# Kernel optimization log

Hardware: AMD Instinct MI355X
Metric: run time of the kernel (lower is better)

## Reference

```python
import jax, jax.numpy as jnp
import numpy as np

H = 256
EDGE_DIM = 16
B, N = 8, 4096
E = 524288
EPS = 1e-5


def setup_inputs() -> dict:
    key = jax.random.key(0)
    ks = jax.random.split(key, 16)
    s = 0.02
    return {
        "h": jax.random.normal(ks[0], (B, N, H), dtype=jnp.float32),
        "edge_index": jax.random.randint(ks[1], (2, E), 0, B * N, dtype=jnp.int64),
        "edge_attr": jax.random.normal(ks[2], (E, EDGE_DIM), dtype=jnp.float32),
        "mask": jnp.ones((B, N), dtype=jnp.float32),
        # message_net params
        "W1": jax.random.normal(ks[3], (2 * H + EDGE_DIM, H), dtype=jnp.float32) * s,
        "b1": jnp.zeros((H,), dtype=jnp.float32),
        "W2": jax.random.normal(ks[4], (H, H), dtype=jnp.float32) * s,
        "b2": jnp.zeros((H,), dtype=jnp.float32),
        # update_net params
        "U1": jax.random.normal(ks[5], (2 * H, H), dtype=jnp.float32) * s,
        "c1": jnp.zeros((H,), dtype=jnp.float32),
        "U2": jax.random.normal(ks[6], (H, H), dtype=jnp.float32) * s,
        "c2": jnp.zeros((H,), dtype=jnp.float32),
        # LayerNorm params
        "gamma": jnp.ones((H,), dtype=jnp.float32),
        "beta": jnp.zeros((H,), dtype=jnp.float32),
    }


def reference(h, edge_index, edge_attr, mask, W1, b1, W2, b2, U1, c1, U2, c2, gamma, beta):
    batch, n_nodes, hid = h.shape
    h_flat = h.reshape(-1, hid)                       # (B*N, H)
    src, dst = edge_index[0], edge_index[1]
    # gather -> message MLP
    msg_in = jnp.concatenate([h_flat[src], h_flat[dst], edge_attr], axis=-1)  # (E, 2H+16)
    messages = jax.nn.silu(msg_in @ W1 + b1) @ W2 + b2                        # (E, H)
    # scatter-add aggregation by destination node
    aggr = jax.ops.segment_sum(messages, dst, num_segments=batch * n_nodes)   # (B*N, H)
    # update MLP + residual (dropout = identity in eval mode)
    upd_in = jnp.concatenate([h_flat, aggr], axis=-1)                         # (B*N, 2H)
    h_new = h_flat + (jax.nn.silu(upd_in @ U1 + c1) @ U2 + c2)
    # LayerNorm over last dim
    mu = jnp.mean(h_new, axis=-1, keepdims=True)
    var = jnp.mean(jnp.square(h_new - mu), axis=-1, keepdims=True)
    h_new = (h_new - mu) * jax.lax.rsqrt(var + EPS) * gamma + beta
    return h_new.reshape(batch, n_nodes, hid) * mask[..., None]
```

## Files before the change

kernel.cpp:

```cpp
#include <hip/hip_runtime.h>

#define H_DIM 256
#define E_NUM 524288
#define NN    32768
#define K2    512
#define K2S   520
#define SAS   264
#define XS    264
#define NPW   4

typedef unsigned short u16;
typedef unsigned int   u32;
typedef __attribute__((ext_vector_type(8))) short s16x8;
typedef __attribute__((ext_vector_type(4))) float f32x4;
typedef __attribute__((ext_vector_type(2))) float f32x2;
typedef __attribute__((ext_vector_type(4))) unsigned short u16x4;

__device__ __forceinline__ u16 f2b(float x) {
    u32 u = __float_as_uint(x);
    u32 r = (u + 0x7FFFu + ((u >> 16) & 1u)) >> 16;
    return (u16)r;
}
__device__ __forceinline__ float b2f(u16 v) {
    u32 u = ((u32)v) << 16;
    return __uint_as_float(u);
}
__device__ __forceinline__ float fsig(float x) {
    return __builtin_amdgcn_rcpf(1.f + __expf(-x));
}

__global__ __launch_bounds__(256) void k_prep_w(
    const float* __restrict__ W1, const float* __restrict__ W2,
    const float* __restrict__ U1, const float* __restrict__ U2,
    u16* __restrict__ WpqT, u16* __restrict__ W2T,
    u16* __restrict__ U1T, u16* __restrict__ U2T) {
    int idx = blockIdx.x * 256 + threadIdx.x;
    if (idx < 131072) {
        int c = idx >> 8, k = idx & 255;
        float v = (c < 256) ? W1[k * 256 + c] : W1[(256 + k) * 256 + (c - 256)];
        WpqT[idx] = f2b(v);
    } else if (idx < 196608) {
        int i = idx - 131072; int c = i >> 8, k = i & 255;
        W2T[i] = f2b(W2[k * 256 + c]);
    } else if (idx < 327680) {
        int i = idx - 196608; int c = i >> 9, k = i & 511;
        U1T[i] = f2b(U1[(size_t)k * 256 + c]);
    } else if (idx < 393216) {
        int i = idx - 327680; int c = i >> 8, k = i & 255;
        U2T[i] = f2b(U2[k * 256 + c]);
    }
}

__global__ __launch_bounds__(256) void k_hist(const int* __restrict__ eidx,
                                              int* __restrict__ cnt) {
    int i = blockIdx.x * 256 + threadIdx.x;
    if (i < E_NUM) atomicAdd(&cnt[eidx[E_NUM + i]], 1);
}

__global__ __launch_bounds__(256) void k_scan(const int* __restrict__ cnt,
                                              int* __restrict__ base,
                                              int* __restrict__ nxt) {
    __shared__ int wsum[4];
    const int t = threadIdx.x, lane = t & 63, w = t >> 6;
    const int st = t * 128;
    int s = 0;
#pragma unroll 8
    for (int i = 0; i < 128; ++i) s += cnt[st + i];
    int sc = s;
#pragma unroll
    for (int off = 1; off < 64; off <<= 1) {
        int v = __shfl_up(sc, off);
        if (lane >= off) sc += v;
    }
    if (lane == 63) wsum[w] = sc;
    __syncthreads();
    int woff = 0;
    for (int i = 0; i < w; ++i) woff += wsum[i];
    const int excl = woff + sc - s;
    if (t == 255) base[NN] = woff + sc;
    int off = excl;
    for (int i = 0; i < 128; ++i) {
        int v = cnt[st + i];
        base[st + i] = off;
        nxt[st + i] = off;
        off += v;
    }
}

__global__ __launch_bounds__(256) void k_scatter(const int* __restrict__ eidx,
                                                 int* __restrict__ nxt,
                                                 int2* __restrict__ elist) {
    int i = blockIdx.x * 256 + threadIdx.x;
    if (i < E_NUM) {
        int d = eidx[E_NUM + i];
        int p = atomicAdd(&nxt[d], 1);
        elist[p] = make_int2(eidx[i], i);
    }
}

__global__ __launch_bounds__(256, 2) void k_gemm_pq(
    const float* __restrict__ h, const u16* __restrict__ WpqT,
    u16* __restrict__ PQ) {
    __shared__ __align__(16) u16 sA[64 * SAS];
    const int t = threadIdx.x;
    const int rowTile = blockIdx.x >> 1, q = blockIdx.x & 1;
    const int n0 = rowTile * 64;
    {
        const int r = t >> 2, g = t & 3;
        const float* hrow = h + (size_t)(n0 + r) * 256;
        u16* rowp = sA + r * SAS;
#pragma unroll
        for (int j = 0; j < 8; ++j) {
            const int c = g + 4 * j;
            float4 v0 = *reinterpret_cast<const float4*>(hrow + c * 8);
            float4 v1 = *reinterpret_cast<const float4*>(hrow + c * 8 + 4);
            s16x8 o;
            o[0] = (short)f2b(v0.x); o[1] = (short)f2b(v0.y);
            o[2] = (short)f2b(v0.z); o[3] = (short)f2b(v0.w);
            o[4] = (short)f2b(v1.x); o[5] = (short)f2b(v1.y);
            o[6] = (short)f2b(v1.z); o[7] = (short)f2b(v1.w);
            *reinterpret_cast<s16x8*>(rowp + c * 8) = o;
        }
    }
    __syncthreads();
    const int lane = t & 63, wv = t >> 6;
    const int l15 = lane & 15, l4 = lane >> 4;
    const int colBase = wv * 64 + l15;
    const f32x4 z4 = {0.f, 0.f, 0.f, 0.f};
    f32x4 acc[4][4];
#pragma unroll
    for (int m = 0; m < 4; ++m)
#pragma unroll
        for (int n = 0; n < 4; ++n) acc[m][n] = z4;
    {
        const u16* Bb = WpqT + (size_t)(q * 256 + colBase) * 256 + l4 * 8;
        for (int kk = 0; kk < 8; ++kk) {
            s16x8 a[4], b[4];
#pragma unroll
            for (int m = 0; m < 4; ++m)
                a[m] = *reinterpret_cast<const s16x8*>(sA + (m * 16 + l15) * SAS + kk * 32 + l4 * 8);
#pragma unroll
            for (int n = 0; n < 4; ++n)
                b[n] = *reinterpret_cast<const s16x8*>(Bb + (size_t)n * 16 * 256 + kk * 32);
#pragma unroll
            for (int m = 0; m < 4; ++m)
#pragma unroll
                for (int n = 0; n < 4; ++n)
                    acc[m][n] = __builtin_amdgcn_mfma_f32_16x16x32_bf16(a[m], b[n], acc[m][n], 0, 0, 0);
        }
    }
#pragma unroll
    for (int m = 0; m < 4; ++m)
#pragma unroll
        for (int j = 0; j < 4; ++j) {
            const int row = n0 + m * 16 + l4 * 4 + j;
            u16* op = PQ + (size_t)row * 512 + q * 256 + colBase;
#pragma unroll
            for (int n = 0; n < 4; ++n) op[n * 16] = f2b(acc[m][n][j]);
        }
}


#define LDEA(S0, S1, S2, S3, k) do {                                        \
    const int _eid = __builtin_amdgcn_readlane(eeY, (k));                   \
    const float* _ep = ea + (size_t)_eid * 16;                              \
    S0 = *reinterpret_cast<const float4*>(_ep);                             \
    S1 = *reinterpret_cast<const float4*>(_ep + 4);                         \
    S2 = *reinterpret_cast<const float4*>(_ep + 8);                         \
    S3 = *reinterpret_cast<const float4*>(_ep + 12);                        \
} while (0)

__global__ __launch_bounds__(256, 4) void k_aggr(
    const u16* __restrict__ PQ, const int2* __restrict__ elist,
    const int* __restrict__ base, const float* __restrict__ ea,
    const float* __restrict__ W1, const float* __restrict__ b1,
    u16* __restrict__ Sb) {
    const int t = threadIdx.x, lane = t & 63, wv = t >> 6;
    const int c0 = lane * 4;
    f32x2 WrL[16], WrH[16];
#pragma unroll
    for (int k = 0; k < 16; ++k) {
        float4 w = *reinterpret_cast<const float4*>(W1 + (size_t)(512 + k) * 256 + c0);
        WrL[k] = f32x2{w.x, w.y};
        WrH[k] = f32x2{w.z, w.w};
    }
    const float4 b1v = *reinterpret_cast<const float4*>(b1 + c0);

    const int dBase = (blockIdx.x * 4 + wv) * NPW;
    for (int nn = 0; nn < NPW; ++nn) {
        const int d = __builtin_amdgcn_readfirstlane(dBase + nn);
        f32x2 qbL = {b1v.x, b1v.y}, qbH = {b1v.z, b1v.w};
        {
            u16x4 qv = *reinterpret_cast<const u16x4*>(PQ + (size_t)d * 512 + 256 + c0);
            qbL[0] += b2f(qv.x); qbL[1] += b2f(qv.y);
            qbH[0] += b2f(qv.z); qbH[1] += b2f(qv.w);
        }
        const int eBeg = __builtin_amdgcn_readfirstlane(base[d]);
        const int nAll = __builtin_amdgcn_readfirstlane(base[d + 1]) - eBeg;
        f32x2 accL = {0.f, 0.f}, accH = {0.f, 0.f};

        for (int cb = 0; cb < nAll; cb += 64) {
            const int m = min(64, nAll - cb);
            const int2 ee = elist[eBeg + cb + min(lane, m - 1)];
            const int eeX = ee.x, eeY = ee.y;

            auto gather = [&](int idx) -> u16x4 {
                const int s = __builtin_amdgcn_readlane(eeX, idx);
                return *reinterpret_cast<const u16x4*>(PQ + (size_t)s * 512 + c0);
            };
            auto edge_compute = [&](const u16x4& pc, const float4& E0, const float4& E1,
                                    const float4& E2, const float4& E3) {
                f32x2 xL = qbL, xH = qbH;
                xL[0] += b2f(pc.x); xL[1] += b2f(pc.y);
                xH[0] += b2f(pc.z); xH[1] += b2f(pc.w);
                xL = xL + WrL[0]  * E0.x; xH = xH + WrH[0]  * E0.x;
                xL = xL + WrL[1]  * E0.y; xH = xH + WrH[1]  * E0.y;
                xL = xL + WrL[2]  * E0.z; xH = xH + WrH[2]  * E0.z;
                xL = xL + WrL[3]  * E0.w; xH = xH + WrH[3]  * E0.w;
                xL = xL + WrL[4]  * E1.x; xH = xH + WrH[4]  * E1.x;
                xL = xL + WrL[5]  * E1.y; xH = xH + WrH[5]  * E1.y;
                xL = xL + WrL[6]  * E1.z; xH = xH + WrH[6]  * E1.z;
                xL = xL + WrL[7]  * E1.w; xH = xH + WrH[7]  * E1.w;
                xL = xL + WrL[8]  * E2.x; xH = xH + WrH[8]  * E2.x;
                xL = xL + WrL[9]  * E2.y; xH = xH + WrH[9]  * E2.y;
                xL = xL + WrL[10] * E2.z; xH = xH + WrH[10] * E2.z;
                xL = xL + WrL[11] * E2.w; xH = xH + WrH[11] * E2.w;
                xL = xL + WrL[12] * E3.x; xH = xH + WrH[12] * E3.x;
                xL = xL + WrL[13] * E3.y; xH = xH + WrH[13] * E3.y;
                xL = xL + WrL[14] * E3.z; xH = xH + WrH[14] * E3.z;
                xL = xL + WrL[15] * E3.w; xH = xH + WrH[15] * E3.w;
                accL[0] += xL[0] * fsig(xL[0]);
                accL[1] += xL[1] * fsig(xL[1]);
                accH[0] += xH[0] * fsig(xH[0]);
                accH[1] += xH[1] * fsig(xH[1]);
            };

            u16x4 p0 = gather(0), p1 = gather(1), p2 = gather(2), p3 = gather(3);
            float4 A0, A1, A2, A3, B0, B1, B2, B3;
            LDEA(A0, A1, A2, A3, 0);
            LDEA(B0, B1, B2, B3, min(1, 63));
            int kb = 0;
            for (; kb + 4 <= m; kb += 4) {
                edge_compute(p0, A0, A1, A2, A3);
                LDEA(A0, A1, A2, A3, min(kb + 2, 63));
                p0 = gather(min(kb + 4, 63));
                edge_compute(p1, B0, B1, B2, B3);
                LDEA(B0, B1, B2, B3, min(kb + 3, 63));
                p1 = gather(min(kb + 5, 63));
                edge_compute(p2, A0, A1, A2, A3);
                LDEA(A0, A1, A2, A3, min(kb + 4, 63));
                p2 = gather(min(kb + 6, 63));
                edge_compute(p3, B0, B1, B2, B3);
                LDEA(B0, B1, B2, B3, min(kb + 5, 63));
                p3 = gather(min(kb + 7, 63));
            }
            if (kb + 0 < m) edge_compute(p0, A0, A1, A2, A3);
            if (kb + 1 < m) edge_compute(p1, B0, B1, B2, B3);
            if (kb + 2 < m) {
                LDEA(A0, A1, A2, A3, kb + 2);
                edge_compute(p2, A0, A1, A2, A3);
            }
        }
        u16x4 o;
        o.x = f2b(accL[0]); o.y = f2b(accL[1]);
        o.z = f2b(accH[0]); o.w = f2b(accH[1]);
        *reinterpret_cast<u16x4*>(Sb + (size_t)d * 256 + c0) = o;
    }
}

__global__ __launch_bounds__(256, 2) void k_post(
    const float* __restrict__ h, const u16* __restrict__ Sb,
    const u16* __restrict__ W2T, const int* __restrict__ base,
    const float* __restrict__ b2,
    const u16* __restrict__ U1T, const u16* __restrict__ U2T,
    const float* __restrict__ c1, const float* __restrict__ c2,
    const float* __restrict__ gamma, const float* __restrict__ beta,
    const float* __restrict__ mask,
    float* __restrict__ out) {
    __shared__ __align__(16) char smemraw[64 * XS * 4];
    u16* sA = reinterpret_cast<u16*>(smemraw);
    const int t  = threadIdx.x;
    const int n0 = blockIdx.x * 64;

    {
        const int r = t >> 2, g = t & 3;
        const int node = n0 + r;
        const float* hrow = h + (size_t)node * H_DIM;
        const u16* srow = Sb + (size_t)node * H_DIM;
        u16* rowp = sA + r * K2S;
#pragma unroll
        for (int j = 0; j < 16; ++j) {
            const int c = g + 4 * j;
            if (c < 32) {
                float4 v0 = *reinterpret_cast<const float4*>(hrow + c * 8);
                float4 v1 = *reinterpret_cast<const float4*>(hrow + c * 8 + 4);
                s16x8 o;
                o[0] = (short)f2b(v0.x); o[1] = (short)f2b(v0.y);
                o[2] = (short)f2b(v0.z); o[3] = (short)f2b(v0.w);
                o[4] = (short)f2b(v1.x); o[5] = (short)f2b(v1.y);
                o[6] = (short)f2b(v1.z); o[7] = (short)f2b(v1.w);
                *reinterpret_cast<s16x8*>(rowp + c * 8) = o;
            } else {
                const int cc = c - 32;
                *reinterpret_cast<s16x8*>(rowp + 256 + cc * 8) =
                    *reinterpret_cast<const s16x8*>(srow + cc * 8);
            }
        }
    }
    __syncthreads();

    const int lane = t & 63, wv = t >> 6;
    const int l15 = lane & 15, l4 = lane >> 4;
    const int colBase = wv * 64 + l15;
    const f32x4 z4 = {0.f, 0.f, 0.f, 0.f};

    f32x4 acc[4][4];
#pragma unroll
    for (int m = 0; m < 4; ++m)
#pragma unroll
        for (int n = 0; n < 4; ++n) acc[m][n] = z4;

    {
        const u16* Bb = W2T + (size_t)colBase * 256 + l4 * 8;
        for (int kk = 0; kk < 8; ++kk) {
            s16x8 a[4], b[4];
#pragma unroll
            for (int m = 0; m < 4; ++m)
                a[m] = *reinterpret_cast<const s16x8*>(sA + (m * 16 + l15) * K2S + 256 + kk * 32 + l4 * 8);
#pragma unroll
            for (int n = 0; n < 4; ++n)
                b[n] = *reinterpret_cast<const s16x8*>(Bb + (size_t)n * 16 * 256 + kk * 32);
#pragma unroll
            for (int m = 0; m < 4; ++m)
#pragma unroll
                for (int n = 0; n < 4; ++n)
                    acc[m][n] = __builtin_amdgcn_mfma_f32_16x16x32_bf16(a[m], b[n], acc[m][n], 0, 0, 0);
        }
    }
    __syncthreads();

    {
        float b2v[4];
#pragma unroll
        for (int n = 0; n < 4; ++n) b2v[n] = b2[colBase + n * 16];
#pragma unroll
        for (int m = 0; m < 4; ++m)
#pragma unroll
            for (int j = 0; j < 4; ++j) {
                const int row = m * 16 + l4 * 4 + j;
                const float dv = (float)(base[n0 + row + 1] - base[n0 + row]);
#pragma unroll
                for (int n = 0; n < 4; ++n)
                    sA[row * K2S + 256 + colBase + n * 16] = f2b(acc[m][n][j] + dv * b2v[n]);
            }
    }
    __syncthreads();

#pragma unroll
    for (int m = 0; m < 4; ++m)
#pragma unroll
        for (int n = 0; n < 4; ++n) acc[m][n] = z4;
    {
        const u16* Bb = U1T + (size_t)colBase * K2 + l4 * 8;
        for (int kk = 0; kk < 16; ++kk) {
            s16x8 a[4], b[4];
#pragma unroll
            for (int m = 0; m < 4; ++m)
                a[m] = *reinterpret_cast<const s16x8*>(sA + (m * 16 + l15) * K2S + kk * 32 + l4 * 8);
#pragma unroll
            for (int n = 0; n < 4; ++n)
                b[n] = *reinterpret_cast<const s16x8*>(Bb + (size_t)n * 16 * K2 + kk * 32);
#pragma unroll
            for (int m = 0; m < 4; ++m)
#pragma unroll
                for (int n = 0; n < 4; ++n)
                    acc[m][n] = __builtin_amdgcn_mfma_f32_16x16x32_bf16(a[m], b[n], acc[m][n], 0, 0, 0);
        }
    }
    __syncthreads();

    {
        u16* sX = reinterpret_cast<u16*>(smemraw);
        float c1v[4];
#pragma unroll
        for (int n = 0; n < 4; ++n) c1v[n] = c1[colBase + n * 16];
#pragma unroll
        for (int m = 0; m < 4; ++m)
#pragma unroll
            for (int n = 0; n < 4; ++n)
#pragma unroll
                for (int j = 0; j < 4; ++j) {
                    float x = acc[m][n][j] + c1v[n];
                    float s = x * fsig(x);
                    sX[(m * 16 + l4 * 4 + j) * XS + colBase + n * 16] = f2b(s);
                }
    }
    __syncthreads();

#pragma unroll
    for (int m = 0; m < 4; ++m)
#pragma unroll
        for (int n = 0; n < 4; ++n) acc[m][n] = z4;
    {
        const u16* sX = reinterpret_cast<u16*>(smemraw);
        const u16* Bb = U2T + (size_t)colBase * H_DIM + l4 * 8;
        for (int kk = 0; kk < 8; ++kk) {
            s16x8 a[4], b[4];
#pragma unroll
            for (int m = 0; m < 4; ++m)
                a[m] = *reinterpret_cast<const s16x8*>(sX + (m * 16 + l15) * XS + kk * 32 + l4 * 8);
#pragma unroll
            for (int n = 0; n < 4; ++n)
                b[n] = *reinterpret_cast<const s16x8*>(Bb + (size_t)n * 16 * H_DIM + kk * 32);
#pragma unroll
            for (int m = 0; m < 4; ++m)
#pragma unroll
                for (int n = 0; n < 4; ++n)
                    acc[m][n] = __builtin_amdgcn_mfma_f32_16x16x32_bf16(a[m], b[n], acc[m][n], 0, 0, 0);
        }
    }
    __syncthreads();

    {
        float* sF = reinterpret_cast<float*>(smemraw);
        float c2v[4];
#pragma unroll
        for (int n = 0; n < 4; ++n) c2v[n] = c2[colBase + n * 16];
#pragma unroll
        for (int m = 0; m < 4; ++m)
#pragma unroll
            for (int n = 0; n < 4; ++n)
#pragma unroll
                for (int j = 0; j < 4; ++j) {
                    const int row = m * 16 + l4 * 4 + j;
                    const float hv = h[(size_t)(n0 + row) * H_DIM + colBase + n * 16];
                    sF[row * XS + colBase + n * 16] = acc[m][n][j] + c2v[n] + hv;
                }
    }
    __syncthreads();

    {
        const float* sF = reinterpret_cast<const float*>(smemraw);
        const int rr = t >> 2, p = t & 3;
        const float* rowf = sF + rr * XS + p * 64;
        float s1 = 0.f, s2 = 0.f;
#pragma unroll
        for (int i = 0; i < 64; ++i) { float v = rowf[i]; s1 += v; s2 += v * v; }
        s1 += __shfl_xor(s1, 1); s1 += __shfl_xor(s1, 2);
        s2 += __shfl_xor(s2, 1); s2 += __shfl_xor(s2, 2);
        const float mu   = s1 * (1.f / 256.f);
        const float var  = s2 * (1.f / 256.f) - mu * mu;
        const float rstd = rsqrtf(var + 1e-5f);
        const int node = n0 + rr;
        const float mk = mask[node];
        float* op = out + (size_t)node * H_DIM + p * 64;
        const float* gp = gamma + p * 64;
        const float* bp = beta + p * 64;
#pragma unroll
        for (int i = 0; i < 64; i += 4) {
            float4 x  = *reinterpret_cast<const float4*>(rowf + i);
            float4 g4 = *reinterpret_cast<const float4*>(gp + i);
            float4 b4 = *reinterpret_cast<const float4*>(bp + i);
            float4 o;
            o.x = (((x.x - mu) * rstd) * g4.x + b4.x) * mk;
            o.y = (((x.y - mu) * rstd) * g4.y + b4.y) * mk;
            o.z = (((x.z - mu) * rstd) * g4.z + b4.z) * mk;
            o.w = (((x.w - mu) * rstd) * g4.w + b4.w) * mk;
            *reinterpret_cast<float4*>(op + i) = o;
        }
    }
}

#define OFF_PQ     0ull
#define OFF_SB     33554432ull
#define OFF_WPQT   50331648ull
#define OFF_W2T    50593792ull
#define OFF_U1T    50724864ull
#define OFF_U2T    50987008ull
#define OFF_CNT    51118080ull
#define OFF_BASE   51249152ull
#define OFF_NEXT   51380480ull
#define OFF_ELIST  51511552ull

extern "C" void kernel_launch(void* const* d_in, const int* in_sizes, int n_in,
                              void* d_out, int out_size, void* d_ws, size_t ws_size,
                              hipStream_t stream) {
    const float* h     = (const float*)d_in[0];
    const int*   eidx  = (const int*)d_in[1];
    const float* ea    = (const float*)d_in[2];
    const float* mask  = (const float*)d_in[3];
    const float* W1    = (const float*)d_in[4];
    const float* b1    = (const float*)d_in[5];
    const float* W2    = (const float*)d_in[6];
    const float* b2    = (const float*)d_in[7];
    const float* U1    = (const float*)d_in[8];
    const float* c1    = (const float*)d_in[9];
    const float* U2    = (const float*)d_in[10];
    const float* c2    = (const float*)d_in[11];
    const float* gamma = (const float*)d_in[12];
    const float* beta  = (const float*)d_in[13];
    float* out = (float*)d_out;
    char*  ws  = (char*)d_ws;

    u16*  PQ    = (u16*)(ws + OFF_PQ);
    u16*  Sb    = (u16*)(ws + OFF_SB);
    u16*  WpqT  = (u16*)(ws + OFF_WPQT);
    u16*  W2T   = (u16*)(ws + OFF_W2T);
    u16*  U1T   = (u16*)(ws + OFF_U1T);
    u16*  U2T   = (u16*)(ws + OFF_U2T);
    int*  cnt   = (int*)(ws + OFF_CNT);
    int*  base  = (int*)(ws + OFF_BASE);
    int*  nxt   = (int*)(ws + OFF_NEXT);
    int2* elist = (int2*)(ws + OFF_ELIST);

    hipMemsetAsync(cnt, 0, (size_t)NN * sizeof(int), stream);

    k_prep_w<<<1536, 256, 0, stream>>>(W1, W2, U1, U2, WpqT, W2T, U1T, U2T);
    k_hist<<<E_NUM / 256, 256, 0, stream>>>(eidx, cnt);
    k_scan<<<1, 256, 0, stream>>>(cnt, base, nxt);
    k_scatter<<<E_NUM / 256, 256, 0, stream>>>(eidx, nxt, elist);
    k_gemm_pq<<<(NN / 64) * 2, 256, 0, stream>>>(h, WpqT, PQ);
    k_aggr<<<NN / (4 * NPW), 256, 0, stream>>>(PQ, elist, base, ea, W1, b1, Sb);
    k_post<<<NN / 64, 256, 0, stream>>>(h, Sb, W2T, base, b2, U1T, U2T,
                                        c1, c2, gamma, beta, mask, out);
}
```

Measured before the change: 285.0 us.

## Pre-sort edge attributes by destination and use one node per wave in aggregation

The scatter kernel now copies each edge's 16-float attribute row into a destination-sorted buffer, so the aggregation kernel reads edge attributes contiguously instead of through an indirect edge id. The edge list shrinks to source ids only. The aggregation kernel also processes one destination node per wave instead of four, launching four times more blocks for finer load balance across uneven degrees. This adds an extra 32 MB write plus read of edge attributes in the scatter pass and a larger workspace.

After: 283.2 us. Within noise of the previous version (-0.6%).

```diff
diff --git a/kernel.cpp b/kernel.cpp
--- a/kernel.cpp
+++ b/kernel.cpp
@@ -7,7 +7,6 @@
 #define K2S   520
 #define SAS   264
 #define XS    264
-#define NPW   4
 
 typedef unsigned short u16;
 typedef unsigned int   u32;
@@ -89,12 +88,18 @@
 
 __global__ __launch_bounds__(256) void k_scatter(const int* __restrict__ eidx,
                                                  int* __restrict__ nxt,
-                                                 int2* __restrict__ elist) {
+                                                 int* __restrict__ elist,
+                                                 float* __restrict__ eas,
+                                                 const float* __restrict__ ea) {
     int i = blockIdx.x * 256 + threadIdx.x;
     if (i < E_NUM) {
         int d = eidx[E_NUM + i];
         int p = atomicAdd(&nxt[d], 1);
-        elist[p] = make_int2(eidx[i], i);
+        elist[p] = eidx[i];
+        const float4* s = reinterpret_cast<const float4*>(ea + (size_t)i * 16);
+        float4* o = reinterpret_cast<float4*>(eas + (size_t)p * 16);
+        float4 v0 = s[0], v1 = s[1], v2 = s[2], v3 = s[3];
+        o[0] = v0; o[1] = v1; o[2] = v2; o[3] = v3;
     }
 }
 
@@ -162,8 +167,7 @@
 
 
 #define LDEA(S0, S1, S2, S3, k) do {                                        \
-    const int _eid = __builtin_amdgcn_readlane(eeY, (k));                   \
-    const float* _ep = ea + (size_t)_eid * 16;                              \
+    const float* _ep = eas + (size_t)(eBeg + cb + min((k), m - 1)) * 16;    \
     S0 = *reinterpret_cast<const float4*>(_ep);                             \
     S1 = *reinterpret_cast<const float4*>(_ep + 4);                         \
     S2 = *reinterpret_cast<const float4*>(_ep + 8);                         \
@@ -171,8 +175,8 @@
 } while (0)
 
 __global__ __launch_bounds__(256, 4) void k_aggr(
-    const u16* __restrict__ PQ, const int2* __restrict__ elist,
-    const int* __restrict__ base, const float* __restrict__ ea,
+    const u16* __restrict__ PQ, const int* __restrict__ elist,
+    const int* __restrict__ base, const float* __restrict__ eas,
     const float* __restrict__ W1, const float* __restrict__ b1,
     u16* __restrict__ Sb) {
     const int t = threadIdx.x, lane = t & 63, wv = t >> 6;
@@ -186,86 +190,82 @@
     }
     const float4 b1v = *reinterpret_cast<const float4*>(b1 + c0);
 
-    const int dBase = (blockIdx.x * 4 + wv) * NPW;
-    for (int nn = 0; nn < NPW; ++nn) {
-        const int d = __builtin_amdgcn_readfirstlane(dBase + nn);
-        f32x2 qbL = {b1v.x, b1v.y}, qbH = {b1v.z, b1v.w};
-        {
-            u16x4 qv = *reinterpret_cast<const u16x4*>(PQ + (size_t)d * 512 + 256 + c0);
-            qbL[0] += b2f(qv.x); qbL[1] += b2f(qv.y);
-            qbH[0] += b2f(qv.z); qbH[1] += b2f(qv.w);
-        }
-        const int eBeg = __builtin_amdgcn_readfirstlane(base[d]);
-        const int nAll = __builtin_amdgcn_readfirstlane(base[d + 1]) - eBeg;
-        f32x2 accL = {0.f, 0.f}, accH = {0.f, 0.f};
-
-        for (int cb = 0; cb < nAll; cb += 64) {
-            const int m = min(64, nAll - cb);
-            const int2 ee = elist[eBeg + cb + min(lane, m - 1)];
-            const int eeX = ee.x, eeY = ee.y;
-
-            auto gather = [&](int idx) -> u16x4 {
-                const int s = __builtin_amdgcn_readlane(eeX, idx);
-                return *reinterpret_cast<const u16x4*>(PQ + (size_t)s * 512 + c0);
-            };
-            auto edge_compute = [&](const u16x4& pc, const float4& E0, const float4& E1,
-                                    const float4& E2, const float4& E3) {
-                f32x2 xL = qbL, xH = qbH;
-                xL[0] += b2f(pc.x); xL[1] += b2f(pc.y);
-                xH[0] += b2f(pc.z); xH[1] += b2f(pc.w);
-                xL = xL + WrL[0]  * E0.x; xH = xH + WrH[0]  * E0.x;
-                xL = xL + WrL[1]  * E0.y; xH = xH + WrH[1]  * E0.y;
-                xL = xL + WrL[2]  * E0.z; xH = xH + WrH[2]  * E0.z;
-                xL = xL + WrL[3]  * E0.w; xH = xH + WrH[3]  * E0.w;
-                xL = xL + WrL[4]  * E1.x; xH = xH + WrH[4]  * E1.x;
-                xL = xL + WrL[5]  * E1.y; xH = xH + WrH[5]  * E1.y;
-                xL = xL + WrL[6]  * E1.z; xH = xH + WrH[6]  * E1.z;
-                xL = xL + WrL[7]  * E1.w; xH = xH + WrH[7]  * E1.w;
-                xL = xL + WrL[8]  * E2.x; xH = xH + WrH[8]  * E2.x;
-                xL = xL + WrL[9]  * E2.y; xH = xH + WrH[9]  * E2.y;
-                xL = xL + WrL[10] * E2.z; xH = xH + WrH[10] * E2.z;
-                xL = xL + WrL[11] * E2.w; xH = xH + WrH[11] * E2.w;
-                xL = xL + WrL[12] * E3.x; xH = xH + WrH[12] * E3.x;
-                xL = xL + WrL[13] * E3.y; xH = xH + WrH[13] * E3.y;
-                xL = xL + WrL[14] * E3.z; xH = xH + WrH[14] * E3.z;
-                xL = xL + WrL[15] * E3.w; xH = xH + WrH[15] * E3.w;
-                accL[0] += xL[0] * fsig(xL[0]);
-                accL[1] += xL[1] * fsig(xL[1]);
-                accH[0] += xH[0] * fsig(xH[0]);
-                accH[1] += xH[1] * fsig(xH[1]);
-            };
-
-            u16x4 p0 = gather(0), p1 = gather(1), p2 = gather(2), p3 = gather(3);
-            float4 A0, A1, A2, A3, B0, B1, B2, B3;
-            LDEA(A0, A1, A2, A3, 0);
-            LDEA(B0, B1, B2, B3, min(1, 63));
-            int kb = 0;
-            for (; kb + 4 <= m; kb += 4) {
-                edge_compute(p0, A0, A1, A2, A3);
-                LDEA(A0, A1, A2, A3, min(kb + 2, 63));
-                p0 = gather(min(kb + 4, 63));
-                edge_compute(p1, B0, B1, B2, B3);
-                LDEA(B0, B1, B2, B3, min(kb + 3, 63));
-                p1 = gather(min(kb + 5, 63));
-                edge_compute(p2, A0, A1, A2, A3);
-                LDEA(A0, A1, A2, A3, min(kb + 4, 63));
-                p2 = gather(min(kb + 6, 63));
-                edge_compute(p3, B0, B1, B2, B3);
-                LDEA(B0, B1, B2, B3, min(kb + 5, 63));
-                p3 = gather(min(kb + 7, 63));
-            }
-            if (kb + 0 < m) edge_compute(p0, A0, A1, A2, A3);
-            if (kb + 1 < m) edge_compute(p1, B0, B1, B2, B3);
-            if (kb + 2 < m) {
-                LDEA(A0, A1, A2, A3, kb + 2);
-                edge_compute(p2, A0, A1, A2, A3);
-            }
-        }
-        u16x4 o;
-        o.x = f2b(accL[0]); o.y = f2b(accL[1]);
-        o.z = f2b(accH[0]); o.w = f2b(accH[1]);
-        *reinterpret_cast<u16x4*>(Sb + (size_t)d * 256 + c0) = o;
-    }
+    const int d = __builtin_amdgcn_readfirstlane(blockIdx.x * 4 + wv);
+    f32x2 qbL = {b1v.x, b1v.y}, qbH = {b1v.z, b1v.w};
+    {
+        u16x4 qv = *reinterpret_cast<const u16x4*>(PQ + (size_t)d * 512 + 256 + c0);
+        qbL[0] += b2f(qv.x); qbL[1] += b2f(qv.y);
+        qbH[0] += b2f(qv.z); qbH[1] += b2f(qv.w);
+    }
+    const int eBeg = __builtin_amdgcn_readfirstlane(base[d]);
+    const int nAll = __builtin_amdgcn_readfirstlane(base[d + 1]) - eBeg;
+    f32x2 accL = {0.f, 0.f}, accH = {0.f, 0.f};
+
+    for (int cb = 0; cb < nAll; cb += 64) {
+        const int m = min(64, nAll - cb);
+        const int eeX = elist[eBeg + cb + min(lane, m - 1)];
+
+        auto gather = [&](int idx) -> u16x4 {
+            const int s = __builtin_amdgcn_readlane(eeX, idx);
+            return *reinterpret_cast<const u16x4*>(PQ + (size_t)s * 512 + c0);
+        };
+        auto edge_compute = [&](const u16x4& pc, const float4& E0, const float4& E1,
+                                const float4& E2, const float4& E3) {
+            f32x2 xL = qbL, xH = qbH;
+            xL[0] += b2f(pc.x); xL[1] += b2f(pc.y);
+            xH[0] += b2f(pc.z); xH[1] += b2f(pc.w);
+            xL = xL + WrL[0]  * E0.x; xH = xH + WrH[0]  * E0.x;
+            xL = xL + WrL[1]  * E0.y; xH = xH + WrH[1]  * E0.y;
+            xL = xL + WrL[2]  * E0.z; xH = xH + WrH[2]  * E0.z;
+            xL = xL + WrL[3]  * E0.w; xH = xH + WrH[3]  * E0.w;
+            xL = xL + WrL[4]  * E1.x; xH = xH + WrH[4]  * E1.x;
+            xL = xL + WrL[5]  * E1.y; xH = xH + WrH[5]  * E1.y;
+            xL = xL + WrL[6]  * E1.z; xH = xH + WrH[6]  * E1.z;
+            xL = xL + WrL[7]  * E1.w; xH = xH + WrH[7]  * E1.w;
+            xL = xL + WrL[8]  * E2.x; xH = xH + WrH[8]  * E2.x;
+            xL = xL + WrL[9]  * E2.y; xH = xH + WrH[9]  * E2.y;
+            xL = xL + WrL[10] * E2.z; xH = xH + WrH[10] * E2.z;
+            xL = xL + WrL[11] * E2.w; xH = xH + WrH[11] * E2.w;
+            xL = xL + WrL[12] * E3.x; xH = xH + WrH[12] * E3.x;
+            xL = xL + WrL[13] * E3.y; xH = xH + WrH[13] * E3.y;
+            xL = xL + WrL[14] * E3.z; xH = xH + WrH[14] * E3.z;
+            xL = xL + WrL[15] * E3.w; xH = xH + WrH[15] * E3.w;
+            accL[0] += xL[0] * fsig(xL[0]);
+            accL[1] += xL[1] * fsig(xL[1]);
+            accH[0] += xH[0] * fsig(xH[0]);
+            accH[1] += xH[1] * fsig(xH[1]);
+        };
+
+        u16x4 p0 = gather(0), p1 = gather(1), p2 = gather(2), p3 = gather(3);
+        float4 A0, A1, A2, A3, B0, B1, B2, B3;
+        LDEA(A0, A1, A2, A3, 0);
+        LDEA(B0, B1, B2, B3, 1);
+        int kb = 0;
+        for (; kb + 4 <= m; kb += 4) {
+            edge_compute(p0, A0, A1, A2, A3);
+            LDEA(A0, A1, A2, A3, kb + 2);
+            p0 = gather(min(kb + 4, 63));
+            edge_compute(p1, B0, B1, B2, B3);
+            LDEA(B0, B1, B2, B3, kb + 3);
+            p1 = gather(min(kb + 5, 63));
+            edge_compute(p2, A0, A1, A2, A3);
+            LDEA(A0, A1, A2, A3, kb + 4);
+            p2 = gather(min(kb + 6, 63));
+            edge_compute(p3, B0, B1, B2, B3);
+            LDEA(B0, B1, B2, B3, kb + 5);
+            p3 = gather(min(kb + 7, 63));
+        }
+        if (kb + 0 < m) edge_compute(p0, A0, A1, A2, A3);
+        if (kb + 1 < m) edge_compute(p1, B0, B1, B2, B3);
+        if (kb + 2 < m) {
+            LDEA(A0, A1, A2, A3, kb + 2);
+            edge_compute(p2, A0, A1, A2, A3);
+        }
+    }
+    u16x4 o;
+    o.x = f2b(accL[0]); o.y = f2b(accL[1]);
+    o.z = f2b(accH[0]); o.w = f2b(accH[1]);
+    *reinterpret_cast<u16x4*>(Sb + (size_t)d * 256 + c0) = o;
 }
 
 __global__ __launch_bounds__(256, 2) void k_post(
@@ -473,14 +473,15 @@
 
 #define OFF_PQ     0ull
 #define OFF_SB     33554432ull
-#define OFF_WPQT   50331648ull
-#define OFF_W2T    50593792ull
-#define OFF_U1T    50724864ull
-#define OFF_U2T    50987008ull
-#define OFF_CNT    51118080ull
-#define OFF_BASE   51249152ull
-#define OFF_NEXT   51380480ull
-#define OFF_ELIST  51511552ull
+#define OFF_EAS    50331648ull
+#define OFF_WPQT   83886080ull
+#define OFF_W2T    84148224ull
+#define OFF_U1T    84279296ull
+#define OFF_U2T    84541440ull
+#define OFF_CNT    84672512ull
+#define OFF_BASE   84803584ull
+#define OFF_NEXT   84934912ull
+#define OFF_ELIST  85065984ull
 
 extern "C" void kernel_launch(void* const* d_in, const int* in_sizes, int n_in,
                               void* d_out, int out_size, void* d_ws, size_t ws_size,
@@ -502,25 +503,26 @@
     float* out = (float*)d_out;
     char*  ws  = (char*)d_ws;
 
-    u16*  PQ    = (u16*)(ws + OFF_PQ);
-    u16*  Sb    = (u16*)(ws + OFF_SB);
-    u16*  WpqT  = (u16*)(ws + OFF_WPQT);
-    u16*  W2T   = (u16*)(ws + OFF_W2T);
-    u16*  U1T   = (u16*)(ws + OFF_U1T);
-    u16*  U2T   = (u16*)(ws + OFF_U2T);
-    int*  cnt   = (int*)(ws + OFF_CNT);
-    int*  base  = (int*)(ws + OFF_BASE);
-    int*  nxt   = (int*)(ws + OFF_NEXT);
-    int2* elist = (int2*)(ws + OFF_ELIST);
+    u16*   PQ    = (u16*)(ws + OFF_PQ);
+    u16*   Sb    = (u16*)(ws + OFF_SB);
+    float* eas   = (float*)(ws + OFF_EAS);
+    u16*   WpqT  = (u16*)(ws + OFF_WPQT);
+    u16*   W2T   = (u16*)(ws + OFF_W2T);
+    u16*   U1T   = (u16*)(ws + OFF_U1T);
+    u16*   U2T   = (u16*)(ws + OFF_U2T);
+    int*   cnt   = (int*)(ws + OFF_CNT);
+    int*   base  = (int*)(ws + OFF_BASE);
+    int*   nxt   = (int*)(ws + OFF_NEXT);
+    int*   elist = (int*)(ws + OFF_ELIST);
 
     hipMemsetAsync(cnt, 0, (size_t)NN * sizeof(int), stream);
 
     k_prep_w<<<1536, 256, 0, stream>>>(W1, W2, U1, U2, WpqT, W2T, U1T, U2T);
     k_hist<<<E_NUM / 256, 256, 0, stream>>>(eidx, cnt);
     k_scan<<<1, 256, 0, stream>>>(cnt, base, nxt);
-    k_scatter<<<E_NUM / 256, 256, 0, stream>>>(eidx, nxt, elist);
+    k_scatter<<<E_NUM / 256, 256, 0, stream>>>(eidx, nxt, elist, eas, ea);
     k_gemm_pq<<<(NN / 64) * 2, 256, 0, stream>>>(h, WpqT, PQ);
-    k_aggr<<<NN / (4 * NPW), 256, 0, stream>>>(PQ, elist, base, ea, W1, b1, Sb);
+    k_aggr<<<NN / 4, 256, 0, stream>>>(PQ, elist, base, eas, W1, b1, Sb);
     k_post<<<NN / 64, 256, 0, stream>>>(h, Sb, W2T, base, b2, U1T, U2T,
                                         c1, c2, gamma, beta, mask, out);
 }
```
